# Kernel tuning notes

Measured on AMD Instinct MI355X. Metric: run time of the kernel, lower is better.

## Reference

```python
import jax, jax.numpy as jnp
import numpy as np

N, CIN, COUT, K, CSTYLE, H, W = 8, 512, 512, 3, 512, 64, 64
EPS = 1e-8
SQRT2 = 2.0 ** 0.5


def setup_inputs() -> dict:
    key = jax.random.key(0)
    ks = jax.random.split(key, 5)
    return {
        "x": jax.random.normal(ks[0], (N, CIN, H, W), jnp.float32),
        "style": jax.random.normal(ks[1], (N, CSTYLE), jnp.float32),
        "noise": jax.random.normal(ks[2], (N, 1, H, W), jnp.float32),
        "conv_weight": jax.random.normal(ks[3], (1, COUT, CIN, K, K), jnp.float32),
        "mod_weight": jax.random.normal(ks[4], (CIN, CSTYLE), jnp.float32) / np.float32(np.sqrt(CSTYLE)),
        "mod_bias": jnp.ones((CIN,), jnp.float32),
        "noise_weight": jnp.zeros((1,), jnp.float32),
        "act_bias": jnp.zeros((COUT,), jnp.float32),
    }


def reference(x, style, noise, conv_weight, mod_weight, mod_bias, noise_weight, act_bias):
    n = x.shape[0]
    # style modulation: linear(style) -> per-sample per-in-channel scale (style_bias=0)
    s = style @ mod_weight.T + mod_bias                       # (n, cin)
    # modulate shared weight (1, cout, cin, k, k) -> (n, cout, cin, k, k)
    w = conv_weight * s[:, None, :, None, None]
    # demodulate
    demod = jax.lax.rsqrt(jnp.sum(w * w, axis=(2, 3, 4)) + EPS)  # (n, cout)
    w = w * demod[:, :, None, None, None]
    # grouped conv: groups = batch
    w = w.reshape(n * COUT, CIN, K, K)
    xg = x.reshape(1, n * CIN, H, W)
    out = jax.lax.conv_general_dilated(
        xg, w,
        window_strides=(1, 1),
        padding=[(K // 2, K // 2), (K // 2, K // 2)],
        dimension_numbers=("NCHW", "OIHW", "NCHW"),
        feature_group_count=n,
    )
    out = out.reshape(n, COUT, H, W) * SQRT2
    # noise injection (scalar weight, broadcast noise)
    out = out + noise_weight[0] * noise
    # fused bias + leaky relu (slope 0.2)
    out = jax.nn.leaky_relu(out + act_bias[None, :, None, None], negative_slope=0.2)
    return out
```

## Files before the change

kernel.cpp:

```cpp
#include <hip/hip_runtime.h>
#include <hip/hip_bf16.h>
#include <stdint.h>


typedef __attribute__((ext_vector_type(8))) short short8;
typedef __attribute__((ext_vector_type(4))) float f32x4;
typedef __attribute__((ext_vector_type(16))) float f32x16;
typedef __attribute__((ext_vector_type(4))) unsigned int uint4v;
typedef __attribute__((ext_vector_type(2))) unsigned int uint2v;

__device__ __forceinline__ unsigned short f2bf(float f) {
  unsigned u = __builtin_bit_cast(unsigned, f);
  u += 0x7FFFu + ((u >> 16) & 1u);
  return (unsigned short)(u >> 16);
}

__device__ __forceinline__ void g2l16(const void* g, void* l) {
  __builtin_amdgcn_global_load_lds(
      (const __attribute__((address_space(1))) void*)g,
      (__attribute__((address_space(3))) void*)l, 16, 0, 0);
}

__global__ void k_pre(const float* __restrict__ style, const float* __restrict__ mw,
                      const float* __restrict__ mb, const float* __restrict__ cw,
                      float* __restrict__ s_out, float* __restrict__ wsq) {
  int t = threadIdx.x;
  int b = blockIdx.x;
  if (b < 1024) {
    int wid = b * 4 + (t >> 6);
    int lane = t & 63;
    int n = wid >> 9, ci = wid & 511;
    float sum = 0.f;
#pragma unroll
    for (int i = 0; i < 8; ++i) {
      int k = lane + i * 64;
      sum += style[n * 512 + k] * mw[ci * 512 + k];
    }
#pragma unroll
    for (int off = 32; off; off >>= 1) sum += __shfl_xor(sum, off, 64);
    if (lane == 0) s_out[wid] = sum + mb[ci];
  } else {
    int id = (b - 1024) * 256 + t;
    const float* p = cw + (size_t)id * 9;
    float a = 0.f;
#pragma unroll
    for (int j = 0; j < 9; ++j) a += p[j] * p[j];
    wsq[id] = a;
  }
}

__global__ void k_mid(const float* __restrict__ s, const float* __restrict__ wsq,
                      const float* __restrict__ x, const float* __restrict__ cw,
                      float* __restrict__ demod, unsigned short* __restrict__ Xp,
                      unsigned short* __restrict__ Wt) {
  __shared__ char smem[74240];
  int t = threadIdx.x;
  int b = blockIdx.x;
  if (b < 512) {
    int n = b >> 6, h = b & 63;
    short* ldsx = (short*)smem;
    float* sxf = (float*)(smem + 69632);
    sxf[t] = s[n * 512 + t];
    sxf[t + 256] = s[n * 512 + 256 + t];
    __syncthreads();
    const float* xb = x + ((size_t)n * 512) * 4096 + h * 64;
#pragma unroll
    for (int i = 0; i < 32; ++i) {
      int L = t + i * 256;
      int ci = L >> 4, q = L & 15;
      f32x4 v = *(const f32x4*)(xb + (size_t)ci * 4096 + q * 4);
      float sv = sxf[ci];
      uint2v o;
      o.x = f2bf(v.x * sv) | ((unsigned)f2bf(v.y * sv) << 16);
      o.y = f2bf(v.z * sv) | ((unsigned)f2bf(v.w * sv) << 16);
      *(uint2v*)(ldsx + ci * 68 + q * 4) = o;
    }
    __syncthreads();
    unsigned short* nb = Xp + (size_t)n * 2230272 + (size_t)(h + 1) * 33792;
#pragma unroll
    for (int r = 0; r < 16; ++r) {
      int u = t + r * 256;
      int cig = u >> 6, col = u & 63;
      unsigned v[8];
#pragma unroll
      for (int j = 0; j < 8; ++j)
        v[j] = (unsigned short)ldsx[(cig * 8 + j) * 68 + col];
      uint4v o;
      o.x = v[0] | (v[1] << 16);
      o.y = v[2] | (v[3] << 16);
      o.z = v[4] | (v[5] << 16);
      o.w = v[6] | (v[7] << 16);
      *(uint4v*)(nb + ((size_t)cig * 66 + col + 1) * 8) = o;
    }
  } else if (b < 1536) {
    int wid = (b - 512) * 4 + (t >> 6);
    int lane = t & 63;
    int n = wid >> 9, co = wid & 511;
    float sum = 0.f;
#pragma unroll
    for (int i = 0; i < 8; ++i) {
      int ci = lane + i * 64;
      float sv = s[n * 512 + ci];
      sum += sv * sv * wsq[co * 512 + ci];
    }
#pragma unroll
    for (int off = 32; off; off >>= 1) sum += __shfl_xor(sum, off, 64);
    if (lane == 0) demod[wid] = rsqrtf(sum + 1e-8f) * 1.41421356237309515f;
  } else if (b < 1792) {
    int bb = b - 1536;
    int cb = bb >> 4, kb = bb & 15;
    float* ldsf = (float*)smem;
#pragma unroll
    for (int i = 0; i < 36; ++i) {
      int idx = t + i * 256;
      int seg = idx / 288, off = idx - seg * 288;
      ldsf[seg * 289 + off] = cw[(size_t)(cb * 32 + seg) * 4608 + kb * 288 + off];
    }
    __syncthreads();
    unsigned short* ob = Wt + (size_t)(cb * 16 + kb) * 9216;
#pragma unroll
    for (int i = 0; i < 5; ++i) {
      int c = t + i * 256;
      if (c < 1152) {
        int co_rel = c & 31, lhi = (c >> 5) & 3, tap = c >> 7;
        unsigned v[8];
#pragma unroll
        for (int j = 0; j < 8; ++j)
          v[j] = f2bf(ldsf[co_rel * 289 + (lhi * 8 + j) * 9 + tap]);
        uint4v o;
        o.x = v[0] | (v[1] << 16);
        o.y = v[2] | (v[3] << 16);
        o.z = v[4] | (v[5] << 16);
        o.w = v[6] | (v[7] << 16);
        *(uint4v*)(ob + (size_t)c * 8) = o;
      }
    }
  } else {
    int bb = b - 1792;
    int n = bb / 17, part = bb % 17;
    uint4v z = (uint4v){0u, 0u, 0u, 0u};
    unsigned short* base = Xp + (size_t)n * 2230272;
#pragma unroll
    for (int i = 0; i < 4; ++i) {
      int id = part * 1024 + i * 256 + t;
      if (id < 16640) {
        size_t off;
        if (id < 8448) {
          int row = (id < 4224) ? 0 : 65;
          int c = id - ((id < 4224) ? 0 : 4224);
          off = (size_t)row * 33792 + (size_t)c * 8;
        } else {
          int id2 = id - 8448;
          int row = 1 + (id2 >> 7);
          int rem = id2 & 127;
          int klhi = rem >> 1;
          int col = (rem & 1) ? 65 : 0;
          off = (size_t)row * 33792 + ((size_t)klhi * 66 + col) * 8;
        }
        *(uint4v*)(base + off) = z;
      }
    }
  }
}

__global__ void __launch_bounds__(256, 2) k_conv(
    const unsigned short* __restrict__ Wt, const unsigned short* __restrict__ Xp,
    const float* __restrict__ demod, const float* __restrict__ noise,
    const float* __restrict__ nw_p, const float* __restrict__ act_bias,
    float* __restrict__ out) {
  __shared__ short lds_a[18432];
  __shared__ short lds_x[22528];
  int t = threadIdx.x;
  int wg = blockIdx.x;
  int n = wg & 7;
  int rem = wg >> 3;
  int rx = rem & 7;
  int cb = rem >> 3;
  int r0 = rx * 8;
  int lane = t & 63, wv = t >> 6;
  int l31 = lane & 31, hi = lane >> 5;
  int ch = wv & 1, rg = wv >> 1;

  const char* ab0 = (const char*)(Wt + (size_t)((cb * 2) * 16) * 9216);
  const char* ab1 = (const char*)(Wt + (size_t)((cb * 2 + 1) * 16) * 9216);
  const unsigned short* xbase = Xp + (size_t)n * 2230272;
  int xoffg[11];
#pragma unroll
  for (int j = 0; j < 11; ++j) {
    int c = j * 256 + t;
    int r = c / 264, rc = c - r * 264;
    int off = (r0 + r) * 33792 + rc * 8;
    if (c >= 2640) off = 0;
    xoffg[j] = off;
  }

  f32x16 acc[2][4];
#pragma unroll
  for (int m = 0; m < 2; ++m)
#pragma unroll
    for (int r = 0; r < 4; ++r)
#pragma unroll
      for (int q = 0; q < 16; ++q) acc[m][r][q] = 0.f;

  const int aoff = hi * 256 + l31 * 8;
  const int xb0 = hi * 528 + ch * 256 + l31 * 8;

  for (int kb = 0; kb < 16; ++kb) {
    __syncthreads();
#pragma unroll
    for (int i = 0; i < 9; ++i) {
      int c = i * 256 + t;
      const char* src = (c < 1152) ? (ab0 + (size_t)kb * 18432 + c * 16)
                                   : (ab1 + (size_t)kb * 18432 + (c - 1152) * 16);
      g2l16(src, (char*)lds_a + c * 16);
    }
#pragma unroll
    for (int j = 0; j < 11; ++j)
      g2l16(xbase + xoffg[j] + kb * 2112, (char*)lds_x + j * 4096 + t * 16);
    __syncthreads();

#pragma unroll
    for (int dw = 0; dw < 3; ++dw) {
      short8 bf[6][2];
#pragma unroll
      for (int rr = 0; rr < 6; ++rr)
#pragma unroll
        for (int ks = 0; ks < 2; ++ks)
          bf[rr][ks] = *(const short8*)(lds_x + (rg * 4 + rr) * 2112 + ks * 1056 +
                                        dw * 8 + xb0);
#pragma unroll
      for (int dh = 0; dh < 3; ++dh) {
        int tap = dh * 3 + dw;
#pragma unroll
        for (int ks = 0; ks < 2; ++ks) {
#pragma unroll
          for (int m = 0; m < 2; ++m) {
            short8 af = *(const short8*)(lds_a + m * 9216 + tap * 1024 + ks * 512 + aoff);
#pragma unroll
            for (int r = 0; r < 4; ++r)
              acc[m][r] = __builtin_amdgcn_mfma_f32_32x32x16_bf16(af, bf[r + dh][ks],
                                                                  acc[m][r], 0, 0, 0);
          }
        }
      }
    }
  }

  float nw = nw_p[0];
  int col = ch * 32 + l31;
  f32x4 dm4[2][4], ab4[2][4];
#pragma unroll
  for (int m = 0; m < 2; ++m)
#pragma unroll
    for (int q = 0; q < 4; ++q) {
      dm4[m][q] = *(const f32x4*)(demod + n * 512 + cb * 64 + m * 32 + q * 8 + hi * 4);
      ab4[m][q] = *(const f32x4*)(act_bias + cb * 64 + m * 32 + q * 8 + hi * 4);
    }
#pragma unroll
  for (int r = 0; r < 4; ++r) {
    int R = r0 + rg * 4 + r;
    float nz = nw * noise[((size_t)n * 64 + R) * 64 + col];
#pragma unroll
    for (int m = 0; m < 2; ++m) {
#pragma unroll
      for (int q = 0; q < 4; ++q) {
#pragma unroll
        for (int c = 0; c < 4; ++c) {
          int co = cb * 64 + m * 32 + q * 8 + hi * 4 + c;
          float v = dm4[m][q][c] * acc[m][r][q * 4 + c] + nz + ab4[m][q][c];
          v = v > 0.f ? v : 0.2f * v;
          out[(((size_t)n * 512 + co) * 64 + R) * 64 + col] = v;
        }
      }
    }
  }
}

extern "C" void kernel_launch(void* const* d_in, const int* in_sizes, int n_in,
                              void* d_out, int out_size, void* d_ws, size_t ws_size,
                              hipStream_t stream) {
  const float* x     = (const float*)d_in[0];
  const float* style = (const float*)d_in[1];
  const float* noise = (const float*)d_in[2];
  const float* cw    = (const float*)d_in[3];
  const float* mw    = (const float*)d_in[4];
  const float* mb    = (const float*)d_in[5];
  const float* nw    = (const float*)d_in[6];
  const float* ab    = (const float*)d_in[7];
  float* out = (float*)d_out;

  char* ws = (char*)d_ws;
  float* s_buf  = (float*)ws;
  float* demod  = (float*)(ws + 16384);
  float* wsq    = (float*)(ws + 32768);
  unsigned short* Wt = (unsigned short*)(ws + 1081344);
  unsigned short* Xp = (unsigned short*)(ws + 5799936);

  k_pre<<<2048, 256, 0, stream>>>(style, mw, mb, cw, s_buf, wsq);
  k_mid<<<1928, 256, 0, stream>>>(s_buf, wsq, x, cw, demod, Xp, Wt);
  k_conv<<<512, 256, 0, stream>>>(Wt, Xp, demod, noise, nw, ab, out);
}
```

Measured before the change: 258.2 us.

## Double-buffer LDS tiles in conv kernel to overlap loads with MFMA

Allocates two LDS buffers for the weight and input tiles and prefetches the next K-block while computing on the current one, with one barrier per iteration instead of two. Launch bounds drop to one block per CU because LDS use doubles. This trades occupancy-based latency hiding for explicit software pipelining within a block.

```diff
diff --git a/kernel.cpp b/kernel.cpp
--- a/kernel.cpp
+++ b/kernel.cpp
@@ -163,13 +163,13 @@
   }
 }
 
-__global__ void __launch_bounds__(256, 2) k_conv(
+__global__ void __launch_bounds__(256, 1) k_conv(
     const unsigned short* __restrict__ Wt, const unsigned short* __restrict__ Xp,
     const float* __restrict__ demod, const float* __restrict__ noise,
     const float* __restrict__ nw_p, const float* __restrict__ act_bias,
     float* __restrict__ out) {
-  __shared__ short lds_a[18432];
-  __shared__ short lds_x[22528];
+  __shared__ short lds_a[2][18432];
+  __shared__ short lds_x[2][22528];
   int t = threadIdx.x;
   int wg = blockIdx.x;
   int n = wg & 7;
@@ -205,20 +205,35 @@
   const int aoff = hi * 256 + l31 * 8;
   const int xb0 = hi * 528 + ch * 256 + l31 * 8;
 
+#pragma unroll
+  for (int i = 0; i < 9; ++i) {
+    int c = i * 256 + t;
+    const char* src = (c < 1152) ? (ab0 + c * 16) : (ab1 + (c - 1152) * 16);
+    g2l16(src, (char*)lds_a[0] + c * 16);
+  }
+#pragma unroll
+  for (int j = 0; j < 11; ++j)
+    g2l16(xbase + xoffg[j], (char*)lds_x[0] + j * 4096 + t * 16);
+  __syncthreads();
+
+  int cur = 0;
   for (int kb = 0; kb < 16; ++kb) {
-    __syncthreads();
-#pragma unroll
-    for (int i = 0; i < 9; ++i) {
-      int c = i * 256 + t;
-      const char* src = (c < 1152) ? (ab0 + (size_t)kb * 18432 + c * 16)
-                                   : (ab1 + (size_t)kb * 18432 + (c - 1152) * 16);
-      g2l16(src, (char*)lds_a + c * 16);
-    }
-#pragma unroll
-    for (int j = 0; j < 11; ++j)
-      g2l16(xbase + xoffg[j] + kb * 2112, (char*)lds_x + j * 4096 + t * 16);
-    __syncthreads();
-
+    if (kb < 15) {
+      int kn = kb + 1;
+#pragma unroll
+      for (int i = 0; i < 9; ++i) {
+        int c = i * 256 + t;
+        const char* src = (c < 1152) ? (ab0 + (size_t)kn * 18432 + c * 16)
+                                     : (ab1 + (size_t)kn * 18432 + (c - 1152) * 16);
+        g2l16(src, (char*)lds_a[cur ^ 1] + c * 16);
+      }
+#pragma unroll
+      for (int j = 0; j < 11; ++j)
+        g2l16(xbase + xoffg[j] + kn * 2112, (char*)lds_x[cur ^ 1] + j * 4096 + t * 16);
+    }
+
+    const short* la = lds_a[cur];
+    const short* lx = lds_x[cur];
 #pragma unroll
     for (int dw = 0; dw < 3; ++dw) {
       short8 bf[6][2];
@@ -226,7 +241,7 @@
       for (int rr = 0; rr < 6; ++rr)
 #pragma unroll
         for (int ks = 0; ks < 2; ++ks)
-          bf[rr][ks] = *(const short8*)(lds_x + (rg * 4 + rr) * 2112 + ks * 1056 +
+          bf[rr][ks] = *(const short8*)(lx + (rg * 4 + rr) * 2112 + ks * 1056 +
                                         dw * 8 + xb0);
 #pragma unroll
       for (int dh = 0; dh < 3; ++dh) {
@@ -235,7 +250,7 @@
         for (int ks = 0; ks < 2; ++ks) {
 #pragma unroll
           for (int m = 0; m < 2; ++m) {
-            short8 af = *(const short8*)(lds_a + m * 9216 + tap * 1024 + ks * 512 + aoff);
+            short8 af = *(const short8*)(la + m * 9216 + tap * 1024 + ks * 512 + aoff);
 #pragma unroll
             for (int r = 0; r < 4; ++r)
               acc[m][r] = __builtin_amdgcn_mfma_f32_32x32x16_bf16(af, bf[r + dh][ks],
@@ -244,6 +259,9 @@
         }
       }
     }
+
+    __syncthreads();
+    cur ^= 1;
   }
 
   float nw = nw_p[0];
```

Measured after the change: 266.7 us. 1.03x slower.

## Double-buffer conv K-chunks in LDS, halving chunk size to overlap loads

Applied to the files above, without the earlier changes.

The conv main loop is split into 32 half-size K phases, each staged into one of two LDS buffers, so global-to-LDS loads for the next phase are issued before the MFMAs on the current phase run. The weight pre-pack kernel is reordered to a (ks, tap, hi) layout so each half-chunk is contiguous. This removes the per-iteration stall where all waves waited on loads, and drops one of the two barriers per step. The cost is more loop iterations, smaller MFMA batches per barrier, and the same total LDS footprint.

```diff
diff --git a/kernel.cpp b/kernel.cpp
--- a/kernel.cpp
+++ b/kernel.cpp
@@ -122,11 +122,16 @@
     for (int i = 0; i < 5; ++i) {
       int c = t + i * 256;
       if (c < 1152) {
-        int co_rel = c & 31, lhi = (c >> 5) & 3, tap = c >> 7;
+        int co_rel = c & 31;
+        int u = c >> 5;
+        int hi = u & 1;
+        int u2 = u >> 1;
+        int ks = (u2 >= 9) ? 1 : 0;
+        int tap = u2 - ks * 9;
         unsigned v[8];
 #pragma unroll
         for (int j = 0; j < 8; ++j)
-          v[j] = f2bf(ldsf[co_rel * 289 + (lhi * 8 + j) * 9 + tap]);
+          v[j] = f2bf(ldsf[co_rel * 289 + (ks * 16 + hi * 8 + j) * 9 + tap]);
         uint4v o;
         o.x = v[0] | (v[1] << 16);
         o.y = v[2] | (v[3] << 16);
@@ -168,8 +173,8 @@
     const float* __restrict__ demod, const float* __restrict__ noise,
     const float* __restrict__ nw_p, const float* __restrict__ act_bias,
     float* __restrict__ out) {
-  __shared__ short lds_a[18432];
-  __shared__ short lds_x[22528];
+  __shared__ short lds_a2[2][9216];
+  __shared__ short lds_x2[2][10560];
   int t = threadIdx.x;
   int wg = blockIdx.x;
   int n = wg & 7;
@@ -184,14 +189,17 @@
   const char* ab0 = (const char*)(Wt + (size_t)((cb * 2) * 16) * 9216);
   const char* ab1 = (const char*)(Wt + (size_t)((cb * 2 + 1) * 16) * 9216);
   const unsigned short* xbase = Xp + (size_t)n * 2230272;
-  int xoffg[11];
-#pragma unroll
-  for (int j = 0; j < 11; ++j) {
+
+  int xoff2[6];
+#pragma unroll
+  for (int j = 0; j < 6; ++j) {
     int c = j * 256 + t;
-    int r = c / 264, rc = c - r * 264;
-    int off = (r0 + r) * 33792 + rc * 8;
-    if (c >= 2640) off = 0;
-    xoffg[j] = off;
+    if (c < 1320) {
+      int r = c / 132, rc = c - r * 132;
+      xoff2[j] = (r0 + r) * 33792 + rc * 8;
+    } else {
+      xoff2[j] = 0;
+    }
   }
 
   f32x16 acc[2][4];
@@ -205,45 +213,57 @@
   const int aoff = hi * 256 + l31 * 8;
   const int xb0 = hi * 528 + ch * 256 + l31 * 8;
 
-  for (int kb = 0; kb < 16; ++kb) {
-    __syncthreads();
-#pragma unroll
-    for (int i = 0; i < 9; ++i) {
+  auto stage = [&](int p, int bi) {
+    int kb = p >> 1, ks = p & 1;
+    size_t abyte = (size_t)kb * 18432 + (size_t)ks * 9216;
+#pragma unroll
+    for (int i = 0; i < 5; ++i) {
       int c = i * 256 + t;
-      const char* src = (c < 1152) ? (ab0 + (size_t)kb * 18432 + c * 16)
-                                   : (ab1 + (size_t)kb * 18432 + (c - 1152) * 16);
-      g2l16(src, (char*)lds_a + c * 16);
-    }
-#pragma unroll
-    for (int j = 0; j < 11; ++j)
-      g2l16(xbase + xoffg[j] + kb * 2112, (char*)lds_x + j * 4096 + t * 16);
-    __syncthreads();
-
+      if (c < 1152) {
+        const char* src = (c < 576) ? (ab0 + abyte + (size_t)c * 16)
+                                    : (ab1 + abyte + (size_t)(c - 576) * 16);
+        g2l16(src, (char*)lds_a2[bi] + c * 16);
+      }
+    }
+    int xadd = kb * 2112 + ks * 1056;
+#pragma unroll
+    for (int j = 0; j < 6; ++j) {
+      int c = j * 256 + t;
+      if (c < 1320)
+        g2l16(xbase + xoff2[j] + xadd, (char*)lds_x2[bi] + c * 16);
+    }
+  };
+
+  stage(0, 0);
+  __syncthreads();
+
+  int cur = 0;
+  for (int p = 0; p < 32; ++p) {
+    if (p < 31) stage(p + 1, cur ^ 1);
+
+    const short* la = lds_a2[cur];
+    const short* lx = lds_x2[cur];
 #pragma unroll
     for (int dw = 0; dw < 3; ++dw) {
-      short8 bf[6][2];
+      short8 bf[6];
 #pragma unroll
       for (int rr = 0; rr < 6; ++rr)
-#pragma unroll
-        for (int ks = 0; ks < 2; ++ks)
-          bf[rr][ks] = *(const short8*)(lds_x + (rg * 4 + rr) * 2112 + ks * 1056 +
-                                        dw * 8 + xb0);
+        bf[rr] = *(const short8*)(lx + (rg * 4 + rr) * 1056 + dw * 8 + xb0);
 #pragma unroll
       for (int dh = 0; dh < 3; ++dh) {
         int tap = dh * 3 + dw;
 #pragma unroll
-        for (int ks = 0; ks < 2; ++ks) {
-#pragma unroll
-          for (int m = 0; m < 2; ++m) {
-            short8 af = *(const short8*)(lds_a + m * 9216 + tap * 1024 + ks * 512 + aoff);
-#pragma unroll
-            for (int r = 0; r < 4; ++r)
-              acc[m][r] = __builtin_amdgcn_mfma_f32_32x32x16_bf16(af, bf[r + dh][ks],
-                                                                  acc[m][r], 0, 0, 0);
-          }
+        for (int m = 0; m < 2; ++m) {
+          short8 af = *(const short8*)(la + m * 4608 + tap * 512 + aoff);
+#pragma unroll
+          for (int r = 0; r < 4; ++r)
+            acc[m][r] = __builtin_amdgcn_mfma_f32_32x32x16_bf16(af, bf[r + dh],
+                                                                acc[m][r], 0, 0, 0);
         }
       }
     }
+    __syncthreads();
+    cur ^= 1;
   }
 
   float nw = nw_p[0];
```

After: 269.0 us. +4.2%, slower.
